# Optimization experiments

Measured on AMD Instinct MI355X. Metric: run time of the kernel, lower is better.

Reference implementation:

```python
import jax, jax.numpy as jnp
import numpy as np

B_BLK = 64      # sparse_block_size
LOCAL = 4       # sparse_local_num_blocks
GLOB = 2        # sparse_global_num_blocks
STRIDE = 4      # sparse_global_block_stride
NH = 16
NKV = 4
HD = 128
SCALE = HD ** -0.5
NEG = -1e9


def _build_block_index(num_blocks):
    """Static per-query-block key-block index table + validity mask."""
    max_sel = LOCAL + 1 + GLOB
    idx = np.zeros((num_blocks, max_sel), np.int32)
    valid = np.zeros((num_blocks, max_sel), bool)
    for t in range(num_blocks):
        local = list(range(max(0, t - LOCAL), t + 1))
        cand = list(range(0, t + 1, max(1, STRIDE)))
        glob = cand[-GLOB:] if (GLOB > 0 and len(cand) > 0) else []
        sel = sorted(set(local + glob))
        idx[t, :len(sel)] = sel
        valid[t, :len(sel)] = True
    return idx, valid


def _rotate_half(x):
    x1, x2 = jnp.split(x, 2, axis=-1)
    return jnp.concatenate((-x2, x1), axis=-1)


def setup_inputs() -> dict:
    key = jax.random.key(0)
    ks = jax.random.split(key, 7)
    bsz, S, H = 1, 4096, 2048
    return {
        "hidden_states": jax.random.normal(ks[0], (bsz, S, H), jnp.float32) * 0.02,
        "cos": jax.random.uniform(ks[1], (bsz, S, HD), jnp.float32, -1.0, 1.0),
        "sin": jax.random.uniform(ks[2], (bsz, S, HD), jnp.float32, -1.0, 1.0),
        "wq": jax.random.normal(ks[3], (NH * HD, H), jnp.float32) * 0.02,
        "wk": jax.random.normal(ks[4], (NKV * HD, H), jnp.float32) * 0.02,
        "wv": jax.random.normal(ks[5], (NKV * HD, H), jnp.float32) * 0.02,
        "wo": jax.random.normal(ks[6], (H, NH * HD), jnp.float32) * 0.02,
    }


def reference(hidden_states, cos, sin, wq, wk, wv, wo):
    b, S, H = hidden_states.shape
    # QKV projections (nn.Linear: x @ W.T), split heads -> [b, h, S, d]
    q = (hidden_states @ wq.T).reshape(b, S, NH, HD).transpose(0, 2, 1, 3)
    k = (hidden_states @ wk.T).reshape(b, S, NKV, HD).transpose(0, 2, 1, 3)
    v = (hidden_states @ wv.T).reshape(b, S, NKV, HD).transpose(0, 2, 1, 3)
    # RoPE (cos/sin broadcast over heads)
    c = cos[:, None, :, :]
    s = sin[:, None, :, :]
    q = q * c + _rotate_half(q) * s
    k = k * c + _rotate_half(k) * s
    # GQA: repeat KV heads
    n_rep = NH // NKV
    k = jnp.repeat(k, n_rep, axis=1)
    v = jnp.repeat(v, n_rep, axis=1)
    # Block-sparse local+global attention (S divisible by B_BLK -> no padding)
    T = S // B_BLK
    q_blk = q.reshape(b, NH, T, B_BLK, HD)
    k_blk = k.reshape(b, NH, T, B_BLK, HD)
    v_blk = v.reshape(b, NH, T, B_BLK, HD)
    idx, valid = _build_block_index(T)           # [T, Smax] static
    Smax = idx.shape[1]
    k_sel = k_blk[:, :, idx]                     # [b,h,T,Smax,Bk,d]
    v_sel = v_blk[:, :, idx]
    scores = jnp.einsum('bhtqd,bhtspd->bhtqsp', q_blk, k_sel) * SCALE
    # causal intra-block mask on the diagonal block, -inf on padded slots
    intra = jnp.triu(jnp.full((B_BLK, B_BLK), NEG, jnp.float32), 1)
    is_diag = jnp.asarray(idx == np.arange(T)[:, None], jnp.float32)  # [T,Smax]
    mask = is_diag[:, None, :, None] * intra[None, :, None, :]        # [T,Bq,Smax,Bk]
    mask = mask + jnp.where(jnp.asarray(valid)[:, None, :, None], 0.0, NEG)
    scores = scores + mask[None, None]
    scores = scores.reshape(b, NH, T, B_BLK, Smax * B_BLK)
    probs = jax.nn.softmax(scores, axis=-1)
    out = jnp.einsum('bhtqk,bhtkd->bhtqd', probs,
                     v_sel.reshape(b, NH, T, Smax * B_BLK, HD))
    out = out.reshape(b, NH, S, HD).transpose(0, 2, 1, 3).reshape(b, S, NH * HD)
    return out @ wo.T
```

## Files before the change

kernel.cpp:

```cpp
#include <hip/hip_runtime.h>

typedef unsigned short u16;
typedef short bf16x8 __attribute__((ext_vector_type(8)));
typedef float f32x4 __attribute__((ext_vector_type(4)));

#define S_LEN 4096
#define NHEADS 16
#define NKVH 4
#define HDIM 128
#define HID 2048
#define NQKV 3072

__device__ __forceinline__ u16 f2bf(float x) {
  union { float f; unsigned u; } v; v.f = x;
  unsigned r = v.u + 0x7fffu + ((v.u >> 16) & 1u);
  return (u16)(r >> 16);
}
__device__ __forceinline__ float bf2f(u16 x) {
  union { unsigned u; float f; } v; v.u = ((unsigned)x) << 16;
  return v.f;
}
__device__ __forceinline__ void async16(u16* lds, const u16* g) {
  __builtin_amdgcn_global_load_lds((const __attribute__((address_space(1))) void*)g,
                                   (__attribute__((address_space(3))) void*)lds, 16, 0, 0);
}

__global__ __launch_bounds__(256) void cast_f32_bf16(const float* __restrict__ in,
                                                     u16* __restrict__ out, int n4) {
  int i = blockIdx.x * 256 + threadIdx.x;
  if (i >= n4) return;
  float4 v = ((const float4*)in)[i];
  ushort4 o;
  o.x = f2bf(v.x); o.y = f2bf(v.y); o.z = f2bf(v.z); o.w = f2bf(v.w);
  ((ushort4*)out)[i] = o;
}

template<bool OUT_BF16>
__global__ __launch_bounds__(256) void gemm_bt(const u16* __restrict__ A, const u16* __restrict__ B,
                                               void* __restrict__ Cp, int M, int N, int K) {
  __shared__ __align__(16) u16 As[128 * 64];
  __shared__ __align__(16) u16 Bs[128 * 64];
  const int tid = threadIdx.x;
  const int w = tid >> 6, l = tid & 63;
  const int quad = l >> 4, l16 = l & 15;
  const int bm = blockIdx.x, bn = blockIdx.y;
  const int wr = w & 1, wc = w >> 1;

  const size_t abase = (size_t)bm * 128 * K;
  const size_t bbase = (size_t)bn * 128 * K;

  f32x4 acc[4][4];
  for (int i = 0; i < 4; ++i)
    for (int j = 0; j < 4; ++j) acc[i][j] = f32x4{0.f, 0.f, 0.f, 0.f};

  int sm[4], sc[4];
  for (int j = 0; j < 4; ++j) {
    int slot = (w * 4 + j) * 64 + l;
    sm[j] = slot >> 3;
    sc[j] = (slot & 7) ^ (sm[j] & 7);
  }
  int aoff[2][4], boff[2][4];
  for (int ksi = 0; ksi < 2; ++ksi) {
    int cb = ksi * 4 + quad;
    for (int mt = 0; mt < 4; ++mt) {
      int m = wr * 64 + mt * 16 + l16;
      aoff[ksi][mt] = (m * 8 + (cb ^ (m & 7))) * 8;
      int n = wc * 64 + mt * 16 + l16;
      boff[ksi][mt] = (n * 8 + (cb ^ (n & 7))) * 8;
    }
  }

  for (int kt = 0; kt < K; kt += 64) {
    __syncthreads();
    for (int j = 0; j < 4; ++j) {
      async16(&As[(w * 4 + j) * 64 * 8], A + abase + (size_t)sm[j] * K + kt + sc[j] * 8);
      async16(&Bs[(w * 4 + j) * 64 * 8], B + bbase + (size_t)sm[j] * K + kt + sc[j] * 8);
    }
    __syncthreads();
    for (int ksi = 0; ksi < 2; ++ksi) {
      bf16x8 af[4], bv[4];
      for (int mt = 0; mt < 4; ++mt) {
        af[mt] = *(const bf16x8*)&As[aoff[ksi][mt]];
        bv[mt] = *(const bf16x8*)&Bs[boff[ksi][mt]];
      }
      for (int mt = 0; mt < 4; ++mt)
        for (int nt = 0; nt < 4; ++nt)
          acc[mt][nt] = __builtin_amdgcn_mfma_f32_16x16x32_bf16(af[mt], bv[nt], acc[mt][nt], 0, 0, 0);
    }
  }

  const int row_base = bm * 128 + wr * 64;
  const int col_base = bn * 128 + wc * 64;
  for (int mt = 0; mt < 4; ++mt)
    for (int nt = 0; nt < 4; ++nt) {
      int col = col_base + nt * 16 + l16;
      for (int r = 0; r < 4; ++r) {
        int row = row_base + mt * 16 + quad * 4 + r;
        float v = acc[mt][nt][r];
        if (OUT_BF16) ((u16*)Cp)[(size_t)row * N + col] = f2bf(v);
        else          ((float*)Cp)[(size_t)row * N + col] = v;
      }
    }
}

__global__ __launch_bounds__(256) void rope_scatter(const u16* __restrict__ qkv,
                                                    const float* __restrict__ cosp,
                                                    const float* __restrict__ sinp,
                                                    u16* __restrict__ Q, u16* __restrict__ Kd) {
  int idx = blockIdx.x * 256 + threadIdx.x;
  int d = idx & 63;
  int hh = (idx >> 6) % 20;
  int s = idx / (20 * 64);
  size_t base = (size_t)s * NQKV + hh * 128;
  float x1 = bf2f(qkv[base + d]);
  float x2 = bf2f(qkv[base + d + 64]);
  float c1 = cosp[s * 128 + d], s1 = sinp[s * 128 + d];
  float c2 = cosp[s * 128 + d + 64], s2 = sinp[s * 128 + d + 64];
  float o1 = x1 * c1 - x2 * s1;
  float o2 = x2 * c2 + x1 * s2;
  u16* dst = (hh < NHEADS) ? (Q + ((size_t)hh * S_LEN + s) * HDIM)
                           : (Kd + ((size_t)(hh - NHEADS) * S_LEN + s) * HDIM);
  dst[d] = f2bf(o1);
  dst[d + 64] = f2bf(o2);
}

__global__ __launch_bounds__(256) void vtrans(const u16* __restrict__ qkv, u16* __restrict__ Vt) {
  __shared__ u16 tile[64][65];
  int s0 = blockIdx.x * 64;
  int j0 = blockIdx.y * 64;
  int tid = threadIdx.x;
  for (int it = 0; it < 16; ++it) {
    int lin = it * 256 + tid;
    int sr = lin >> 6, jc = lin & 63;
    tile[sr][jc] = qkv[(size_t)(s0 + sr) * NQKV + 2560 + j0 + jc];
  }
  __syncthreads();
  for (int it = 0; it < 16; ++it) {
    int lin = it * 256 + tid;
    int dr = lin >> 6, sc = lin & 63;
    Vt[(size_t)(j0 + dr) * S_LEN + s0 + sc] = tile[sc][dr];
  }
}

__global__ __launch_bounds__(256) void attn_kernel(const u16* __restrict__ Q, const u16* __restrict__ K,
                                                   const u16* __restrict__ Vt, u16* __restrict__ Aout) {
  const float SCALE = 0.08838834764831845f;
  const float NEGF = -3.0e38f;
  const int t = blockIdx.x, h = blockIdx.y;
  const int kvh = h >> 2;
  const int tid = threadIdx.x;
  const int w = tid >> 6, l = tid & 63, quad = l >> 4, l16 = l & 15;

  __shared__ __align__(16) u16 Qs[64 * 128];
  __shared__ __align__(16) u16 Ks[64 * 128];
  __shared__ __align__(16) u16 Vs[128 * 64];
  __shared__ __align__(16) u16 Ps[4 * 16 * 72];

  int sel[7]; int nsel = 0;
  {
    int g1 = (t >> 2) << 2, g0 = g1 - 4;
    int lo = t - 4; if (lo < 0) lo = 0;
    if (g0 >= 0 && g0 < lo) sel[nsel++] = g0;
    if (g1 < lo) sel[nsel++] = g1;
    for (int b = lo; b <= t; ++b) sel[nsel++] = b;
  }

  {
    const size_t qbase = ((size_t)h * S_LEN + t * 64) * HDIM;
    for (int j = 0; j < 4; ++j) {
      int slot = (w * 4 + j) * 64 + l;
      int m = slot >> 4;
      int c = (slot & 15) ^ (m & 15);
      async16(&Qs[(w * 4 + j) * 64 * 8], Q + qbase + m * 128 + c * 8);
    }
  }

  float m_run[4], l_run[4];
  for (int r = 0; r < 4; ++r) { m_run[r] = NEGF; l_run[r] = 0.f; }
  f32x4 oacc[8];
  for (int i = 0; i < 8; ++i) oacc[i] = f32x4{0.f, 0.f, 0.f, 0.f};

  for (int ib = 0; ib < nsel; ++ib) {
    const int kb = sel[ib];
    __syncthreads();
    {
      const size_t kbase = ((size_t)kvh * S_LEN + kb * 64) * HDIM;
      const size_t vbase = (size_t)kvh * HDIM * S_LEN + kb * 64;
      for (int j = 0; j < 4; ++j) {
        int slot = (w * 4 + j) * 64 + l;
        int mk = slot >> 4;
        int ck = (slot & 15) ^ (mk & 15);
        async16(&Ks[(w * 4 + j) * 64 * 8], K + kbase + mk * 128 + ck * 8);
        int dv = slot >> 3;
        int cv = (slot & 7) ^ (dv & 7);
        async16(&Vs[(w * 4 + j) * 64 * 8], Vt + vbase + (size_t)dv * S_LEN + cv * 8);
      }
    }
    __syncthreads();

    f32x4 sacc[4];
    for (int nt = 0; nt < 4; ++nt) sacc[nt] = f32x4{0.f, 0.f, 0.f, 0.f};
    const int mq = w * 16 + l16;
    for (int ks = 0; ks < 128; ks += 32) {
      int cb = (ks >> 3) + quad;
      bf16x8 af = *(const bf16x8*)&Qs[(mq * 16 + (cb ^ (mq & 15))) * 8];
      for (int nt = 0; nt < 4; ++nt) {
        int n = nt * 16 + l16;
        bf16x8 bv = *(const bf16x8*)&Ks[(n * 16 + (cb ^ (n & 15))) * 8];
        sacc[nt] = __builtin_amdgcn_mfma_f32_16x16x32_bf16(af, bv, sacc[nt], 0, 0, 0);
      }
    }

    const bool diag = (kb == t);
    float alpha[4];
    for (int r = 0; r < 4; ++r) {
      int qrow = w * 16 + quad * 4 + r;
      float pv[4];
      float vmax = NEGF;
      for (int nt = 0; nt < 4; ++nt) {
        float v = sacc[nt][r] * SCALE;
        if (diag && (nt * 16 + l16) > qrow) v = NEGF;
        pv[nt] = v;
        vmax = fmaxf(vmax, v);
      }
      for (int off = 1; off < 16; off <<= 1) vmax = fmaxf(vmax, __shfl_xor(vmax, off));
      float mnew = fmaxf(m_run[r], vmax);
      alpha[r] = __expf(m_run[r] - mnew);
      m_run[r] = mnew;
      float sum = 0.f;
      for (int nt = 0; nt < 4; ++nt) {
        float p = __expf(pv[nt] - mnew);
        sum += p;
        Ps[(w * 16 + quad * 4 + r) * 72 + nt * 16 + l16] = f2bf(p);
      }
      for (int off = 1; off < 16; off <<= 1) sum += __shfl_xor(sum, off);
      l_run[r] = l_run[r] * alpha[r] + sum;
    }
    for (int nt = 0; nt < 8; ++nt) {
      f32x4 o = oacc[nt];
      o[0] *= alpha[0]; o[1] *= alpha[1]; o[2] *= alpha[2]; o[3] *= alpha[3];
      oacc[nt] = o;
    }

    for (int ks = 0; ks < 64; ks += 32) {
      bf16x8 pf = *(const bf16x8*)&Ps[(w * 16 + l16) * 72 + ks + quad * 8];
      int cb = (ks >> 3) + quad;
      for (int nt = 0; nt < 8; ++nt) {
        int n = nt * 16 + l16;
        bf16x8 vv = *(const bf16x8*)&Vs[(n * 8 + (cb ^ (n & 7))) * 8];
        oacc[nt] = __builtin_amdgcn_mfma_f32_16x16x32_bf16(pf, vv, oacc[nt], 0, 0, 0);
      }
    }
  }

  float inv[4];
  for (int r = 0; r < 4; ++r) inv[r] = 1.f / l_run[r];
  const int srow = t * 64 + w * 16 + quad * 4;
  for (int nt = 0; nt < 8; ++nt) {
    int col = h * 128 + nt * 16 + l16;
    for (int r = 0; r < 4; ++r)
      Aout[(size_t)(srow + r) * HID + col] = f2bf(oacc[nt][r] * inv[r]);
  }
}

extern "C" void kernel_launch(void* const* d_in, const int* in_sizes, int n_in,
                              void* d_out, int out_size, void* d_ws, size_t ws_size,
                              hipStream_t stream) {
  const float* hs   = (const float*)d_in[0];
  const float* cosp = (const float*)d_in[1];
  const float* sinp = (const float*)d_in[2];
  const float* wq   = (const float*)d_in[3];
  const float* wk   = (const float*)d_in[4];
  const float* wv   = (const float*)d_in[5];
  const float* wo   = (const float*)d_in[6];

  u16* hsb = (u16*)d_ws;
  u16* W   = hsb + (size_t)S_LEN * HID;
  u16* wob = W + (size_t)NQKV * HID;
  u16* qkv = wob + (size_t)HID * HID;
  u16* Qm  = qkv + (size_t)S_LEN * NQKV;
  u16* Km  = Qm + (size_t)NHEADS * S_LEN * HDIM;
  u16* Vt  = Km + (size_t)NKVH * S_LEN * HDIM;
  u16* att = Vt + (size_t)NKVH * HDIM * S_LEN;

  cast_f32_bf16<<<8192, 256, 0, stream>>>(hs, hsb, 2097152);
  cast_f32_bf16<<<4096, 256, 0, stream>>>(wq, W, 1048576);
  cast_f32_bf16<<<1024, 256, 0, stream>>>(wk, W + (size_t)4194304, 262144);
  cast_f32_bf16<<<1024, 256, 0, stream>>>(wv, W + (size_t)5242880, 262144);
  cast_f32_bf16<<<4096, 256, 0, stream>>>(wo, wob, 1048576);

  gemm_bt<true><<<dim3(32, 24), 256, 0, stream>>>(hsb, W, (void*)qkv, 4096, 3072, 2048);
  rope_scatter<<<20480, 256, 0, stream>>>(qkv, cosp, sinp, Qm, Km);
  vtrans<<<dim3(64, 8), 256, 0, stream>>>(qkv, Vt);
  attn_kernel<<<dim3(64, 16), 256, 0, stream>>>(Qm, Km, Vt, att);
  gemm_bt<false><<<dim3(32, 16), 256, 0, stream>>>(att, wob, d_out, 4096, 2048, 2048);
}
```

Before: 288.3 us.

## Add 256x256 eight-wave pipelined GEMM for QKV projection

Adds a new GEMM kernel that uses 512 threads and 256x256 output tiles. It double-buffers LDS with asynchronous global-to-LDS loads and issues each stage between sub-tile MFMA phases, using explicit waitcnt, barriers and setprio to overlap loads with compute. Only the QKV projection switches to it, which cuts the grid to 192 blocks. That grid may underfill the 256 CUs of MI355X, and the 128 KB of LDS per block limits occupancy.

```diff
diff --git a/kernel.cpp b/kernel.cpp
--- a/kernel.cpp
+++ b/kernel.cpp
@@ -97,6 +97,121 @@
       for (int r = 0; r < 4; ++r) {
         int row = row_base + mt * 16 + quad * 4 + r;
         float v = acc[mt][nt][r];
+        if (OUT_BF16) ((u16*)Cp)[(size_t)row * N + col] = f2bf(v);
+        else          ((float*)Cp)[(size_t)row * N + col] = v;
+      }
+    }
+}
+
+#define VMC4 asm volatile("s_waitcnt vmcnt(4)" ::: "memory")
+#define VMC0 asm volatile("s_waitcnt vmcnt(0)" ::: "memory")
+#define NOVM ((void)0)
+
+#define STAGE_A(buf, h, kt) do { \
+    async16(&As[buf][adst[h][0]], asrc[h][0] + (size_t)(kt) * 64); \
+    async16(&As[buf][adst[h][1]], asrc[h][1] + (size_t)(kt) * 64); \
+  } while (0)
+#define STAGE_B(buf, h, kt) do { \
+    async16(&Bs[buf][bdst[h][0]], bsrc[h][0] + (size_t)(kt) * 64); \
+    async16(&Bs[buf][bdst[h][1]], bsrc[h][1] + (size_t)(kt) * 64); \
+  } while (0)
+
+#define PHASE(cur, mh, nh, STAGE_STMT, VM) do { \
+    bf16x8 af_[4][2], bf_[2][2]; \
+    _Pragma("unroll") \
+    for (int i_ = 0; i_ < 4; ++i_) { \
+      const int m64_ = (wm * 128 + ((mh) * 4 + i_) * 16 + l16) * 64; \
+      af_[i_][0] = *(const bf16x8*)&As[cur][m64_ + ((quad ^ x7) * 8)]; \
+      af_[i_][1] = *(const bf16x8*)&As[cur][m64_ + (((4 + quad) ^ x7) * 8)]; \
+    } \
+    _Pragma("unroll") \
+    for (int i_ = 0; i_ < 2; ++i_) { \
+      const int n64_ = (wn * 64 + ((nh) * 2 + i_) * 16 + l16) * 64; \
+      bf_[i_][0] = *(const bf16x8*)&Bs[cur][n64_ + ((quad ^ x7) * 8)]; \
+      bf_[i_][1] = *(const bf16x8*)&Bs[cur][n64_ + (((4 + quad) ^ x7) * 8)]; \
+    } \
+    STAGE_STMT; \
+    __builtin_amdgcn_s_barrier(); \
+    asm volatile("s_waitcnt lgkmcnt(0)" ::: "memory"); \
+    __builtin_amdgcn_sched_barrier(0); \
+    __builtin_amdgcn_s_setprio(1); \
+    _Pragma("unroll") \
+    for (int ks_ = 0; ks_ < 2; ++ks_) \
+      _Pragma("unroll") \
+      for (int i_ = 0; i_ < 4; ++i_) \
+        _Pragma("unroll") \
+        for (int j_ = 0; j_ < 2; ++j_) \
+          acc[(mh) * 4 + i_][(nh) * 2 + j_] = __builtin_amdgcn_mfma_f32_16x16x32_bf16( \
+              af_[i_][ks_], bf_[j_][ks_], acc[(mh) * 4 + i_][(nh) * 2 + j_], 0, 0, 0); \
+    __builtin_amdgcn_s_setprio(0); \
+    VM; \
+    __builtin_amdgcn_s_barrier(); \
+  } while (0)
+
+template<bool OUT_BF16>
+__global__ __launch_bounds__(512, 2) void gemm8p(const u16* __restrict__ A, const u16* __restrict__ B,
+                                                 void* __restrict__ Cp, int M, int N, int K) {
+  __shared__ __align__(16) u16 As[2][256 * 64];
+  __shared__ __align__(16) u16 Bs[2][256 * 64];
+  const int tid = threadIdx.x;
+  const int w = tid >> 6, l = tid & 63, quad = l >> 4, l16 = l & 15;
+  const int wm = w >> 2, wn = w & 3;
+  const int x7 = l16 & 7;
+  const int bm = blockIdx.x, bn = blockIdx.y;
+
+  const u16* asrc[2][2]; int adst[2][2];
+  const u16* bsrc[2][2]; int bdst[2][2];
+#pragma unroll
+  for (int h = 0; h < 2; ++h)
+#pragma unroll
+    for (int j = 0; j < 2; ++j) {
+      int u = j * 512 + w * 64 + l;
+      int r = u >> 3, cc = u & 7;
+      int ma = ((r >> 6) << 7) + (h << 6) + (r & 63);
+      asrc[h][j] = A + (size_t)(bm * 256 + ma) * K + (size_t)((cc ^ (ma & 7)) * 8);
+      int nb = ((r >> 5) << 6) + (h << 5) + (r & 31);
+      bsrc[h][j] = B + (size_t)(bn * 256 + nb) * K + (size_t)((cc ^ (nb & 7)) * 8);
+      int r0 = j * 64 + w * 8;
+      adst[h][j] = (((r0 >> 6) << 7) + (h << 6) + (r0 & 63)) * 64;
+      bdst[h][j] = (((r0 >> 5) << 6) + (h << 5) + (r0 & 31)) * 64;
+    }
+
+  f32x4 acc[8][4];
+#pragma unroll
+  for (int i = 0; i < 8; ++i)
+#pragma unroll
+    for (int j = 0; j < 4; ++j) acc[i][j] = f32x4{0.f, 0.f, 0.f, 0.f};
+
+  STAGE_A(0, 0, 0); STAGE_B(0, 0, 0); STAGE_B(0, 1, 0); STAGE_A(0, 1, 0);
+  STAGE_A(1, 0, 1); STAGE_B(1, 0, 1);
+  VMC4;
+  __builtin_amdgcn_s_barrier();
+
+  const int NI = K >> 7;
+  for (int it = 0; it < NI; ++it) {
+    const int t1 = 2 * it + 1, t2 = 2 * it + 2, t3 = 2 * it + 3;
+    const bool full = (it + 1 < NI);
+    PHASE(0, 0, 0, STAGE_B(1, 1, t1), NOVM);
+    PHASE(0, 0, 1, STAGE_A(1, 1, t1), NOVM);
+    PHASE(0, 1, 0, if (full) STAGE_A(0, 0, t2), NOVM);
+    PHASE(0, 1, 1, if (full) STAGE_B(0, 0, t2), if (full) VMC4; else VMC0);
+    PHASE(1, 0, 0, if (full) STAGE_B(0, 1, t2), NOVM);
+    PHASE(1, 0, 1, if (full) STAGE_A(0, 1, t2), NOVM);
+    PHASE(1, 1, 0, if (full) STAGE_A(1, 0, t3), NOVM);
+    PHASE(1, 1, 1, if (full) STAGE_B(1, 0, t3), if (full) VMC4);
+  }
+
+  const int row0 = bm * 256 + wm * 128;
+  const int col0 = bn * 256 + wn * 64;
+#pragma unroll
+  for (int mf = 0; mf < 8; ++mf)
+#pragma unroll
+    for (int nf = 0; nf < 4; ++nf) {
+      const int col = col0 + nf * 16 + l16;
+#pragma unroll
+      for (int r = 0; r < 4; ++r) {
+        const int row = row0 + mf * 16 + quad * 4 + r;
+        float v = acc[mf][nf][r];
         if (OUT_BF16) ((u16*)Cp)[(size_t)row * N + col] = f2bf(v);
         else          ((float*)Cp)[(size_t)row * N + col] = v;
       }
@@ -289,7 +404,7 @@
   cast_f32_bf16<<<1024, 256, 0, stream>>>(wv, W + (size_t)5242880, 262144);
   cast_f32_bf16<<<4096, 256, 0, stream>>>(wo, wob, 1048576);
 
-  gemm_bt<true><<<dim3(32, 24), 256, 0, stream>>>(hsb, W, (void*)qkv, 4096, 3072, 2048);
+  gemm8p<true><<<dim3(16, 12), 512, 0, stream>>>(hsb, W, (void*)qkv, 4096, 3072, 2048);
   rope_scatter<<<20480, 256, 0, stream>>>(qkv, cosp, sinp, Qm, Km);
   vtrans<<<dim3(64, 8), 256, 0, stream>>>(qkv, Vt);
   attn_kernel<<<dim3(64, 16), 256, 0, stream>>>(Qm, Km, Vt, att);
```

Measured after the change: 305.3 us. 5.9% more time.
